# Kernel optimization log

Hardware: AMD Instinct MI355X
Metric: run time of the kernel (lower is better)

## Reference

```python
import jax, jax.numpy as jnp
import numpy as np

B, L, Z, H = 8, 256, 16, 256


def setup_inputs() -> dict:
    key = jax.random.key(0)
    k1, k2, k3, k4 = jax.random.split(key, 4)
    start_logits = jax.random.normal(k1, (B, L, H), dtype=jnp.float32)
    end_logits = jax.random.normal(k2, (B, L, H), dtype=jnp.float32)
    cls_logits = jax.random.normal(k3, (B, Z, H), dtype=jnp.float32)
    # nn.init.normal_(std=0.1)
    weight_start_end = 0.1 * jax.random.normal(k4, (H, H, H), dtype=jnp.float32)
    return {
        "start_logits": start_logits,
        "end_logits": end_logits,
        "cls_logits": cls_logits,
        "weight_start_end": weight_start_end,
    }


def reference(start_logits, end_logits, cls_logits, weight_start_end):
    # start: [b,x,i], weight: [i,o,j], end: [b,y,j], cls: [b,z,o]
    # Stage 1a: contract i ->  [b,x,o,j]  (GEMM: (b*x, i) @ (i, o*j))
    sw = jnp.einsum('bxi,ioj->bxoj', start_logits, weight_start_end)
    # Stage 1b: contract j ->  [b,x,y,o]
    start_end = jnp.einsum('bxoj,byj->bxyo', sw, end_logits)
    # Stage 2: contract o ->  [b,x,y,z]
    span_logits = jnp.einsum('bxyo,bzo->bxyz', start_end, cls_logits)
    return span_logits
```

## Files before the change

### kernel.cpp

```cpp
#include <hip/hip_runtime.h>


typedef __attribute__((ext_vector_type(8))) short          bf16x8;
typedef __attribute__((ext_vector_type(8))) unsigned short u16x8;
typedef __attribute__((ext_vector_type(4))) unsigned short u16x4;
typedef __attribute__((ext_vector_type(4))) float          f32x4;

#define LDST 40

__device__ __forceinline__ unsigned short f2bf(float f) {
    unsigned u = __builtin_bit_cast(unsigned, f);
    u += 0x7fff + ((u >> 16) & 1);
    return (unsigned short)(u >> 16);
}

template<bool AB16, bool BB16, bool BTRANS, bool CB16>
__global__ __launch_bounds__(512, 4)
void gemm_mfma(const void* __restrict__ Abv, const void* __restrict__ Bbv,
               void* __restrict__ Cbv,
               int lda, int ldb, int ldc,
               long aBS, int aSh, long bBS, int bSh, long cBS)
{
    __shared__ unsigned short As[2][128 * LDST];
    __shared__ unsigned short Bs[2][128 * LDST];

    const int tid  = threadIdx.x;
    const int bz   = blockIdx.z;
    const int row0 = blockIdx.y * 128;
    const int col0 = blockIdx.x * 128;

    const float*          Af = (const float*)Abv          + (long)(bz >> aSh) * aBS;
    const unsigned short* Ah = (const unsigned short*)Abv + (long)(bz >> aSh) * aBS;
    const float*          Bf = (const float*)Bbv          + (long)(bz >> bSh) * bBS;
    const unsigned short* Bh = (const unsigned short*)Bbv + (long)(bz >> bSh) * bBS;
    float*          Cf = (float*)Cbv          + (long)bz * cBS;
    unsigned short* Ch = (unsigned short*)Cbv + (long)bz * cBS;

    const int ar  = tid >> 2;
    const int akc = tid & 3;
    const int kp  = (tid >> 5) * 2;
    const int ng  = (tid & 31) * 4;

    const int wid = tid >> 6, lane = tid & 63;
    const int wm = wid >> 1, wn = wid & 1;
    const int lr = lane & 15, lg = lane >> 4;

    f32x4 acc[2][4] = {};

    float4 aPf[2]; u16x8 aPh;
    float4 bNf[2]; u16x8 bNh;
    float4 bTf[2]; u16x4 bTh[2];

    auto LOAD = [&](int k0) {
        if constexpr (!AB16) {
            const float* p = Af + (long)(row0 + ar) * lda + k0 + akc * 8;
            aPf[0] = *(const float4*)p;
            aPf[1] = *(const float4*)(p + 4);
        } else {
            aPh = *(const u16x8*)(Ah + (long)(row0 + ar) * lda + k0 + akc * 8);
        }
        if constexpr (!BTRANS) {
            if constexpr (!BB16) {
                const float* p = Bf + (long)(col0 + ar) * ldb + k0 + akc * 8;
                bNf[0] = *(const float4*)p;
                bNf[1] = *(const float4*)(p + 4);
            } else {
                bNh = *(const u16x8*)(Bh + (long)(col0 + ar) * ldb + k0 + akc * 8);
            }
        } else {
            if constexpr (!BB16) {
                const float* p = Bf + (long)(k0 + kp) * ldb + col0 + ng;
                bTf[0] = *(const float4*)p;
                bTf[1] = *(const float4*)(p + ldb);
            } else {
                const unsigned short* p = Bh + (long)(k0 + kp) * ldb + col0 + ng;
                bTh[0] = *(const u16x4*)p;
                bTh[1] = *(const u16x4*)(p + ldb);
            }
        }
    };

    auto WRITE = [&](int buf) {
        u16x8 w;
        if constexpr (!AB16) {
            const float* v = (const float*)&aPf[0];
#pragma unroll
            for (int e = 0; e < 8; ++e) w[e] = f2bf(v[e]);
        } else {
            w = aPh;
        }
        *(u16x8*)(As[buf] + ar * LDST + akc * 8) = w;

        if constexpr (!BTRANS) {
            u16x8 wb;
            if constexpr (!BB16) {
                const float* v = (const float*)&bNf[0];
#pragma unroll
                for (int e = 0; e < 8; ++e) wb[e] = f2bf(v[e]);
            } else {
                wb = bNh;
            }
            *(u16x8*)(Bs[buf] + ar * LDST + akc * 8) = wb;
        } else {
#pragma unroll
            for (int e = 0; e < 4; ++e) {
                unsigned lo, hi;
                if constexpr (!BB16) {
                    const float* v0 = (const float*)&bTf[0];
                    const float* v1 = (const float*)&bTf[1];
                    lo = f2bf(v0[e]); hi = f2bf(v1[e]);
                } else {
                    lo = bTh[0][e]; hi = bTh[1][e];
                }
                *(unsigned*)(Bs[buf] + (ng + e) * LDST + kp) = lo | (hi << 16);
            }
        }
    };

    auto COMPUTE = [&](int buf) {
        bf16x8 aF[2], bF[4];
#pragma unroll
        for (int fm = 0; fm < 2; ++fm)
            aF[fm] = *(const bf16x8*)&As[buf][(wm * 32 + fm * 16 + lr) * LDST + lg * 8];
#pragma unroll
        for (int fn = 0; fn < 4; ++fn)
            bF[fn] = *(const bf16x8*)&Bs[buf][(wn * 64 + fn * 16 + lr) * LDST + lg * 8];
        __builtin_amdgcn_s_setprio(1);
#pragma unroll
        for (int fm = 0; fm < 2; ++fm)
#pragma unroll
            for (int fn = 0; fn < 4; ++fn)
                acc[fm][fn] = __builtin_amdgcn_mfma_f32_16x16x32_bf16(
                    aF[fm], bF[fn], acc[fm][fn], 0, 0, 0);
        __builtin_amdgcn_s_setprio(0);
    };

    LOAD(0);
    WRITE(0);
#pragma unroll
    for (int s = 0; s < 8; ++s) {
        if (s < 7) LOAD((s + 1) * 32);
        asm volatile("s_waitcnt lgkmcnt(0)" ::: "memory");
        __builtin_amdgcn_s_barrier();
        COMPUTE(s & 1);
        if (s < 7) WRITE((s + 1) & 1);
    }

#pragma unroll
    for (int fm = 0; fm < 2; ++fm)
#pragma unroll
        for (int q = 0; q < 4; ++q) {
            const long row = row0 + wm * 32 + fm * 16 + lg * 4 + q;
#pragma unroll
            for (int fn = 0; fn < 4; ++fn) {
                const int col = col0 + wn * 64 + fn * 16 + lr;
                if constexpr (CB16) Ch[row * ldc + col] = f2bf(acc[fm][fn][q]);
                else                Cf[row * ldc + col] = acc[fm][fn][q];
            }
        }
}

__global__ __launch_bounds__(256)
void ztranspose(const float* __restrict__ tmp, float* __restrict__ out)
{
    __shared__ float lds[256][17];
    const int tid = threadIdx.x;
    const int b = blockIdx.x >> 8;
    const int x = blockIdx.x & 255;
    const int w = tid >> 6, l = tid & 63;

#pragma unroll
    for (int rep = 0; rep < 4; ++rep) {
        const int z = rep * 4 + w;
        float4 v = *(const float4*)(tmp + ((long)(b * 16 + z) * 256 + x) * 256 + l * 4);
        lds[l * 4 + 0][z] = v.x;
        lds[l * 4 + 1][z] = v.y;
        lds[l * 4 + 2][z] = v.z;
        lds[l * 4 + 3][z] = v.w;
    }
    __syncthreads();

    float* op = out + (long)(b * 256 + x) * 4096;
#pragma unroll
    for (int q = 0; q < 4; ++q) {
        const int y  = q * 64 + (tid >> 2);
        const int z0 = (tid & 3) * 4;
        float4 v = { lds[y][z0], lds[y][z0 + 1], lds[y][z0 + 2], lds[y][z0 + 3] };
        *(float4*)(op + (q * 256 + tid) * 4) = v;
    }
}

extern "C" void kernel_launch(void* const* d_in, const int* in_sizes, int n_in,
                              void* d_out, int out_size, void* d_ws, size_t ws_size,
                              hipStream_t stream)
{
    const float* start = (const float*)d_in[0];
    const float* endl  = (const float*)d_in[1];
    const float* cls   = (const float*)d_in[2];
    const float* W     = (const float*)d_in[3];
    float* out = (float*)d_out;

    unsigned short* Wc  = (unsigned short*)d_ws;
    unsigned short* T   = (unsigned short*)d_out;
    float*          tmp = (float*)d_ws;

    hipLaunchKernelGGL((gemm_mfma<false, false, true, true>), dim3(2, 1, 256), dim3(512), 0, stream,
        (const void*)cls, (const void*)W, (void*)Wc,
        256, 256, 65536, 0L, 0, 65536L, 0, 256L);

    hipLaunchKernelGGL((gemm_mfma<false, true, true, true>), dim3(2, 2, 128), dim3(512), 0, stream,
        (const void*)start, (const void*)Wc, (void*)T,
        256, 256, 256, 65536L, 4, 65536L, 0, 65536L);

    hipLaunchKernelGGL((gemm_mfma<true, false, false, false>), dim3(2, 2, 128), dim3(512), 0, stream,
        (const void*)T, (const void*)endl, (void*)tmp,
        256, 256, 256, 65536L, 0, 65536L, 4, 65536L);

    hipLaunchKernelGGL(ztranspose, dim3(2048), dim3(256), 0, stream, tmp, out);
}
```

Measured before the change: 158.1 us.

## Fuse final end-contraction GEMM with z-transpose and deepen GEMM load prefetch

The third batched GEMM and the separate z-transpose kernel are replaced by one fused_out kernel. It reads bf16 end logits (converted once by a new cvt_bf16 kernel) and the bf16 intermediate T, then writes the output directly in [b,x,y,z] layout. This removes the fp32 tmp round trip through memory and one launch. The transposing GEMM is specialized, remaps the B-load thread indexing, adds a second register prefetch stage and drops setprio. Risks: fused_out has no LDS reuse, and the output stores are narrow scalar writes.

```diff
diff --git a/kernel.cpp b/kernel.cpp
--- a/kernel.cpp
+++ b/kernel.cpp
@@ -14,12 +14,12 @@
     return (unsigned short)(u >> 16);
 }
 
-template<bool AB16, bool BB16, bool BTRANS, bool CB16>
+template<bool BB16>
 __global__ __launch_bounds__(512, 4)
-void gemm_mfma(const void* __restrict__ Abv, const void* __restrict__ Bbv,
-               void* __restrict__ Cbv,
-               int lda, int ldb, int ldc,
-               long aBS, int aSh, long bBS, int bSh, long cBS)
+void gemm_trans(const float* __restrict__ Ab, const void* __restrict__ Bbv,
+                unsigned short* __restrict__ Cb,
+                int lda, int ldb, int ldc,
+                long aBS, int aSh, long bBS, long cBS)
 {
     __shared__ unsigned short As[2][128 * LDST];
     __shared__ unsigned short Bs[2][128 * LDST];
@@ -29,17 +29,15 @@
     const int row0 = blockIdx.y * 128;
     const int col0 = blockIdx.x * 128;
 
-    const float*          Af = (const float*)Abv          + (long)(bz >> aSh) * aBS;
-    const unsigned short* Ah = (const unsigned short*)Abv + (long)(bz >> aSh) * aBS;
-    const float*          Bf = (const float*)Bbv          + (long)(bz >> bSh) * bBS;
-    const unsigned short* Bh = (const unsigned short*)Bbv + (long)(bz >> bSh) * bBS;
-    float*          Cf = (float*)Cbv          + (long)bz * cBS;
-    unsigned short* Ch = (unsigned short*)Cbv + (long)bz * cBS;
+    const float*          Af = Ab + (long)(bz >> aSh) * aBS;
+    const float*          Bf = (const float*)Bbv          + (long)bz * bBS;
+    const unsigned short* Bh = (const unsigned short*)Bbv + (long)bz * bBS;
+    unsigned short*       C  = Cb + (long)bz * cBS;
 
     const int ar  = tid >> 2;
     const int akc = tid & 3;
-    const int kp  = (tid >> 5) * 2;
-    const int ng  = (tid & 31) * 4;
+    const int kp  = (tid & 15) * 2;
+    const int ng  = (tid >> 4) * 4;
 
     const int wid = tid >> 6, lane = tid & 63;
     const int wm = wid >> 1, wn = wid & 1;
@@ -47,73 +45,43 @@
 
     f32x4 acc[2][4] = {};
 
-    float4 aPf[2]; u16x8 aPh;
-    float4 bNf[2]; u16x8 bNh;
-    float4 bTf[2]; u16x4 bTh[2];
-
-    auto LOAD = [&](int k0) {
-        if constexpr (!AB16) {
-            const float* p = Af + (long)(row0 + ar) * lda + k0 + akc * 8;
-            aPf[0] = *(const float4*)p;
-            aPf[1] = *(const float4*)(p + 4);
+    float4 aP[2][2];
+    float4 bPf[2][2];
+    u16x4  bPh[2][2];
+
+    auto LOAD = [&](int set, int k0) {
+        const float* p = Af + (long)(row0 + ar) * lda + k0 + akc * 8;
+        aP[set][0] = *(const float4*)p;
+        aP[set][1] = *(const float4*)(p + 4);
+        if constexpr (!BB16) {
+            const float* q = Bf + (long)(k0 + kp) * ldb + col0 + ng;
+            bPf[set][0] = *(const float4*)q;
+            bPf[set][1] = *(const float4*)(q + ldb);
         } else {
-            aPh = *(const u16x8*)(Ah + (long)(row0 + ar) * lda + k0 + akc * 8);
+            const unsigned short* q = Bh + (long)(k0 + kp) * ldb + col0 + ng;
+            bPh[set][0] = *(const u16x4*)q;
+            bPh[set][1] = *(const u16x4*)(q + ldb);
         }
-        if constexpr (!BTRANS) {
+    };
+
+    auto WRITE = [&](int set, int buf) {
+        u16x8 w;
+        const float* v = (const float*)&aP[set][0];
+#pragma unroll
+        for (int e = 0; e < 8; ++e) w[e] = f2bf(v[e]);
+        *(u16x8*)(As[buf] + ar * LDST + akc * 8) = w;
+
+#pragma unroll
+        for (int e = 0; e < 4; ++e) {
+            unsigned lo, hi;
             if constexpr (!BB16) {
-                const float* p = Bf + (long)(col0 + ar) * ldb + k0 + akc * 8;
-                bNf[0] = *(const float4*)p;
-                bNf[1] = *(const float4*)(p + 4);
+                const float* v0 = (const float*)&bPf[set][0];
+                const float* v1 = (const float*)&bPf[set][1];
+                lo = f2bf(v0[e]); hi = f2bf(v1[e]);
             } else {
-                bNh = *(const u16x8*)(Bh + (long)(col0 + ar) * ldb + k0 + akc * 8);
+                lo = bPh[set][0][e]; hi = bPh[set][1][e];
             }
-        } else {
-            if constexpr (!BB16) {
-                const float* p = Bf + (long)(k0 + kp) * ldb + col0 + ng;
-                bTf[0] = *(const float4*)p;
-                bTf[1] = *(const float4*)(p + ldb);
-            } else {
-                const unsigned short* p = Bh + (long)(k0 + kp) * ldb + col0 + ng;
-                bTh[0] = *(const u16x4*)p;
-                bTh[1] = *(const u16x4*)(p + ldb);
-            }
-        }
-    };
-
-    auto WRITE = [&](int buf) {
-        u16x8 w;
-        if constexpr (!AB16) {
-            const float* v = (const float*)&aPf[0];
-#pragma unroll
-            for (int e = 0; e < 8; ++e) w[e] = f2bf(v[e]);
-        } else {
-            w = aPh;
-        }
-        *(u16x8*)(As[buf] + ar * LDST + akc * 8) = w;
-
-        if constexpr (!BTRANS) {
-            u16x8 wb;
-            if constexpr (!BB16) {
-                const float* v = (const float*)&bNf[0];
-#pragma unroll
-                for (int e = 0; e < 8; ++e) wb[e] = f2bf(v[e]);
-            } else {
-                wb = bNh;
-            }
-            *(u16x8*)(Bs[buf] + ar * LDST + akc * 8) = wb;
-        } else {
-#pragma unroll
-            for (int e = 0; e < 4; ++e) {
-                unsigned lo, hi;
-                if constexpr (!BB16) {
-                    const float* v0 = (const float*)&bTf[0];
-                    const float* v1 = (const float*)&bTf[1];
-                    lo = f2bf(v0[e]); hi = f2bf(v1[e]);
-                } else {
-                    lo = bTh[0][e]; hi = bTh[1][e];
-                }
-                *(unsigned*)(Bs[buf] + (ng + e) * LDST + kp) = lo | (hi << 16);
-            }
+            *(unsigned*)(Bs[buf] + (ng + e) * LDST + kp) = lo | (hi << 16);
         }
     };
 
@@ -125,25 +93,24 @@
 #pragma unroll
         for (int fn = 0; fn < 4; ++fn)
             bF[fn] = *(const bf16x8*)&Bs[buf][(wn * 64 + fn * 16 + lr) * LDST + lg * 8];
-        __builtin_amdgcn_s_setprio(1);
 #pragma unroll
         for (int fm = 0; fm < 2; ++fm)
 #pragma unroll
             for (int fn = 0; fn < 4; ++fn)
                 acc[fm][fn] = __builtin_amdgcn_mfma_f32_16x16x32_bf16(
                     aF[fm], bF[fn], acc[fm][fn], 0, 0, 0);
-        __builtin_amdgcn_s_setprio(0);
-    };
-
-    LOAD(0);
-    WRITE(0);
+    };
+
+    LOAD(0, 0);
+    WRITE(0, 0);
+    LOAD(1, 32);
 #pragma unroll
     for (int s = 0; s < 8; ++s) {
-        if (s < 7) LOAD((s + 1) * 32);
         asm volatile("s_waitcnt lgkmcnt(0)" ::: "memory");
         __builtin_amdgcn_s_barrier();
+        if (s < 6) LOAD(s & 1, (s + 2) * 32);
         COMPUTE(s & 1);
-        if (s < 7) WRITE((s + 1) & 1);
+        if (s < 7) WRITE((s + 1) & 1, (s + 1) & 1);
     }
 
 #pragma unroll
@@ -154,40 +121,68 @@
 #pragma unroll
             for (int fn = 0; fn < 4; ++fn) {
                 const int col = col0 + wn * 64 + fn * 16 + lr;
-                if constexpr (CB16) Ch[row * ldc + col] = f2bf(acc[fm][fn][q]);
-                else                Cf[row * ldc + col] = acc[fm][fn][q];
+                C[row * (long)ldc + col] = f2bf(acc[fm][fn][q]);
             }
         }
 }
 
 __global__ __launch_bounds__(256)
-void ztranspose(const float* __restrict__ tmp, float* __restrict__ out)
-{
-    __shared__ float lds[256][17];
+void fused_out(const unsigned short* __restrict__ endbf,
+               const unsigned short* __restrict__ T,
+               float* __restrict__ out)
+{
     const int tid = threadIdx.x;
     const int b = blockIdx.x >> 8;
     const int x = blockIdx.x & 255;
-    const int w = tid >> 6, l = tid & 63;
-
-#pragma unroll
-    for (int rep = 0; rep < 4; ++rep) {
-        const int z = rep * 4 + w;
-        float4 v = *(const float4*)(tmp + ((long)(b * 16 + z) * 256 + x) * 256 + l * 4);
-        lds[l * 4 + 0][z] = v.x;
-        lds[l * 4 + 1][z] = v.y;
-        lds[l * 4 + 2][z] = v.z;
-        lds[l * 4 + 3][z] = v.w;
+    const int wid = tid >> 6, lane = tid & 63;
+    const int lr = lane & 15, lg = lane >> 4;
+
+    const unsigned short* Arow = endbf + (long)b * 65536;
+    const unsigned short* Bcol = T + (long)(b * 16 + lr) * 65536 + x * 256;
+
+    f32x4 acc[4] = {};
+    u16x8 a[2][4], bb[2];
+
+    auto LOADF = [&](int set, int k0) {
+#pragma unroll
+        for (int fm = 0; fm < 4; ++fm)
+            a[set][fm] = *(const u16x8*)(Arow + (long)(wid * 64 + fm * 16 + lr) * 256 + k0 + lg * 8);
+        bb[set] = *(const u16x8*)(Bcol + k0 + lg * 8);
+    };
+
+    LOADF(0, 0);
+#pragma unroll
+    for (int s = 0; s < 8; ++s) {
+        if (s < 7) LOADF((s + 1) & 1, (s + 1) * 32);
+#pragma unroll
+        for (int fm = 0; fm < 4; ++fm)
+            acc[fm] = __builtin_amdgcn_mfma_f32_16x16x32_bf16(
+                __builtin_bit_cast(bf16x8, a[s & 1][fm]),
+                __builtin_bit_cast(bf16x8, bb[s & 1]), acc[fm], 0, 0, 0);
     }
-    __syncthreads();
 
     float* op = out + (long)(b * 256 + x) * 4096;
 #pragma unroll
-    for (int q = 0; q < 4; ++q) {
-        const int y  = q * 64 + (tid >> 2);
-        const int z0 = (tid & 3) * 4;
-        float4 v = { lds[y][z0], lds[y][z0 + 1], lds[y][z0 + 2], lds[y][z0 + 3] };
-        *(float4*)(op + (q * 256 + tid) * 4) = v;
-    }
+    for (int fm = 0; fm < 4; ++fm)
+#pragma unroll
+        for (int q = 0; q < 4; ++q)
+            op[(wid * 64 + fm * 16 + lg * 4 + q) * 16 + lr] = acc[fm][q];
+}
+
+__global__ __launch_bounds__(256)
+void cvt_bf16(const float* __restrict__ in, unsigned short* __restrict__ out)
+{
+    const int i = (blockIdx.x * 256 + threadIdx.x) * 8;
+    float4 v0 = *(const float4*)(in + i);
+    float4 v1 = *(const float4*)(in + i + 4);
+    const float* v = (const float*)&v0;
+    u16x8 w;
+#pragma unroll
+    for (int e = 0; e < 4; ++e) w[e] = f2bf(v[e]);
+    const float* u = (const float*)&v1;
+#pragma unroll
+    for (int e = 0; e < 4; ++e) w[4 + e] = f2bf(u[e]);
+    *(u16x8*)(out + i) = w;
 }
 
 extern "C" void kernel_launch(void* const* d_in, const int* in_sizes, int n_in,
@@ -200,21 +195,18 @@
     const float* W     = (const float*)d_in[3];
     float* out = (float*)d_out;
 
-    unsigned short* Wc  = (unsigned short*)d_ws;
-    unsigned short* T   = (unsigned short*)d_out;
-    float*          tmp = (float*)d_ws;
-
-    hipLaunchKernelGGL((gemm_mfma<false, false, true, true>), dim3(2, 1, 256), dim3(512), 0, stream,
-        (const void*)cls, (const void*)W, (void*)Wc,
-        256, 256, 65536, 0L, 0, 65536L, 0, 256L);
-
-    hipLaunchKernelGGL((gemm_mfma<false, true, true, true>), dim3(2, 2, 128), dim3(512), 0, stream,
-        (const void*)start, (const void*)Wc, (void*)T,
-        256, 256, 256, 65536L, 4, 65536L, 0, 65536L);
-
-    hipLaunchKernelGGL((gemm_mfma<true, false, false, false>), dim3(2, 2, 128), dim3(512), 0, stream,
-        (const void*)T, (const void*)endl, (void*)tmp,
-        256, 256, 256, 65536L, 0, 65536L, 4, 65536L);
-
-    hipLaunchKernelGGL(ztranspose, dim3(2048), dim3(256), 0, stream, tmp, out);
-}
+    char* ws = (char*)d_ws;
+    unsigned short* Wc    = (unsigned short*)ws;
+    unsigned short* T     = (unsigned short*)(ws + 16777216);
+    unsigned short* endbf = (unsigned short*)(ws + 33554432);
+
+    hipLaunchKernelGGL(cvt_bf16, dim3(256), dim3(256), 0, stream, endl, endbf);
+
+    hipLaunchKernelGGL((gemm_trans<false>), dim3(2, 1, 256), dim3(512), 0, stream,
+        cls, (const void*)W, Wc, 256, 256, 65536, 0L, 0, 65536L, 256L);
+
+    hipLaunchKernelGGL((gemm_trans<true>), dim3(2, 2, 128), dim3(512), 0, stream,
+        start, (const void*)Wc, T, 256, 256, 256, 65536L, 4, 65536L, 65536L);
+
+    hipLaunchKernelGGL(fused_out, dim3(2048), dim3(256), 0, stream, endbf, T, out);
+}
```

New measurement: 174.5 us. 1.1x slower.
